# Kernel optimization log

Hardware: AMD Instinct MI355X
Metric: run time of the kernel (lower is better)

Reference implementation:

```python
import jax, jax.numpy as jnp
import numpy as np

B, NA, LD, AD = 2048, 8, 256, 256
D = LD + AD            # token_dim = 512
E, K, H = 4, 2, 8      # n_experts, top_k, n_attention_heads
FFN, HEAD, BINS = 2048, 512, 101
DH = D // H
LN_EPS = 1e-5


def setup_inputs() -> dict:
    key = jax.random.key(0)
    ks = jax.random.split(key, 9)
    s = 0.02
    return {
        "latents": jax.random.normal(ks[0], (B, NA, LD), jnp.float32),
        "actions": jax.random.normal(ks[1], (B, NA, AD), jnp.float32),
        "gate_W": jax.random.normal(ks[2], (NA * D, E), jnp.float32) * s,
        "Wqkv": jax.random.normal(ks[3], (E, D, 3 * D), jnp.float32) * s,
        "bqkv": jnp.zeros((E, 3 * D), jnp.float32),
        "Wo": jax.random.normal(ks[4], (E, D, D), jnp.float32) * s,
        "bo": jnp.zeros((E, D), jnp.float32),
        "ln1_g": jnp.ones((E, D), jnp.float32),
        "ln1_b": jnp.zeros((E, D), jnp.float32),
        "Wf1": jax.random.normal(ks[5], (E, D, FFN), jnp.float32) * s,
        "bf1": jnp.zeros((E, FFN), jnp.float32),
        "Wf2": jax.random.normal(ks[6], (E, FFN, D), jnp.float32) * s,
        "bf2": jnp.zeros((E, D), jnp.float32),
        "ln2_g": jnp.ones((E, D), jnp.float32),
        "ln2_b": jnp.zeros((E, D), jnp.float32),
        "head_W1": jax.random.normal(ks[7], (NA * D, HEAD), jnp.float32) * s,
        "head_b1": jnp.zeros((HEAD,), jnp.float32),
        "head_W2": jax.random.normal(ks[8], (HEAD, BINS), jnp.float32) * s,
        "head_b2": jnp.zeros((BINS,), jnp.float32),
    }


def _layernorm(x, g, b):
    mu = x.mean(-1, keepdims=True)
    var = ((x - mu) ** 2).mean(-1, keepdims=True)
    return (x - mu) / jnp.sqrt(var + LN_EPS) * g + b


def _expert(tokens, Wqkv, bqkv, Wo, bo, g1, b1, Wf1, bf1, Wf2, bf2, g2, b2):
    # tokens: [B, N, D] -> self-attention + FFN block (pre-residual, post-LN)
    b, n, d = tokens.shape
    qkv = tokens @ Wqkv + bqkv                                  # [B, N, 3D]
    q, k, v = jnp.split(qkv, 3, axis=-1)
    heads = lambda x: x.reshape(b, n, H, DH).transpose(0, 2, 1, 3)  # [B, H, N, dh]
    q, k, v = heads(q), heads(k), heads(v)
    scores = jnp.einsum("bhqd,bhkd->bhqk", q, k) / np.float32(np.sqrt(DH))
    attn = jax.nn.softmax(scores, axis=-1)
    ctx = jnp.einsum("bhqk,bhkd->bhqd", attn, v).transpose(0, 2, 1, 3).reshape(b, n, d)
    x = _layernorm(tokens + ctx @ Wo + bo, g1, b1)
    h = jax.nn.relu(x @ Wf1 + bf1) @ Wf2 + bf2
    return _layernorm(x + h, g2, b2)


def _cv2(x):
    # coefficient of variation squared (unbiased var, matches torch .var())
    x = x.astype(jnp.float32)
    return jnp.var(x, ddof=1) / (jnp.mean(x) ** 2 + 1e-10)


def reference(latents, actions, gate_W, Wqkv, bqkv, Wo, bo, ln1_g, ln1_b,
              Wf1, bf1, Wf2, bf2, ln2_g, ln2_b, head_W1, head_b1, head_W2, head_b2):
    tokens = jnp.concatenate([latents, actions], axis=-1)       # [B, NA, D]
    flat = tokens.reshape(B, -1)
    # --- router (eval mode: clean logits, no noise) ---
    logits = flat @ gate_W                                      # [B, E]
    topv, topi = jax.lax.top_k(logits, min(K + 1, E))
    gk = jax.nn.softmax(topv[:, :K], axis=1)
    gates = jnp.zeros_like(logits).at[jnp.arange(B)[:, None], topi[:, :K]].set(gk)
    # --- experts: run all densely; zero-gate tokens contribute nothing,
    #     identical math to the original masked dispatch/combine ---
    expert_out = jax.vmap(_expert, in_axes=(None,) + (0,) * 12)(
        tokens, Wqkv, bqkv, Wo, bo, ln1_g, ln1_b, Wf1, bf1, Wf2, bf2, ln2_g, ln2_b)  # [E, B, N, D]
    mixed = jnp.einsum("be,ebnd->bnd", gates, expert_out)
    reward_logits = jax.nn.relu(mixed.reshape(B, -1) @ head_W1 + head_b1) @ head_W2 + head_b2
    # --- aux: load balancing loss ---
    load = (gates > 0).sum(0)
    lbl = _cv2(gates.sum(0)) + _cv2(load) + jnp.mean(jax.nn.logsumexp(logits, axis=-1))
    return reward_logits, gates, lbl
```

## Files before the change

### kernel.cpp

```cpp
#include <hip/hip_runtime.h>
#include <stdint.h>

#define NB    2048
#define NAG   8
#define NEXP  4
#define LN_EPS 1e-5f

#define OUT_GATES  (2048*101)
#define OUT_LBL    (OUT_GATES + 2048*4)

typedef __attribute__((ext_vector_type(8))) short short8;
typedef __attribute__((ext_vector_type(4))) float f32x4;

#define MFMA_BF16(a,b,c) __builtin_amdgcn_mfma_f32_16x16x32_bf16((a),(b),(c),0,0,0)

__device__ __forceinline__ float bf2f(unsigned short h){
  union { unsigned int u; float f; } v; v.u = ((unsigned int)h) << 16; return v.f;
}
__device__ __forceinline__ unsigned short f2bf(float x){
  union { float f; unsigned int u; } v; v.f = x;
  unsigned int r = v.u + 0x7FFFu + ((v.u >> 16) & 1u);
  return (unsigned short)(r >> 16);
}
union bfpack8 { short8 v; unsigned short u[8]; };

__device__ __forceinline__ void gload16(const void* g, void* l){
  __builtin_amdgcn_global_load_lds(
      (const __attribute__((address_space(1))) void*)g,
      (__attribute__((address_space(3))) void*)l, 16, 0, 0);
}

#define OFF_WQKVT  0ULL
#define OFF_WOT    6291456ULL
#define OFF_WF1T   8388608ULL
#define OFF_WF2T   16777216ULL
#define OFF_HW1T   25165824ULL
#define OFF_HW2T   29360128ULL
#define OFF_XBF    29474816ULL
#define OFF_SLOTO  63029248ULL
#define OFF_HID    96583680ULL
#define OFF_JOBS   98680832ULL
#define OFF_SLOTW  98713600ULL
#define OFF_LSE    98729984ULL
#define OFF_CNT    98738176ULL
#define WS_NEED    98738192ULL

__global__ __launch_bounds__(256) void k_transpose_cast(const float* __restrict__ src,
    unsigned short* __restrict__ dst, int R, int C){
  __shared__ float tile[32][33];
  int e = blockIdx.z;
  int c0 = blockIdx.x*32, r0 = blockIdx.y*32;
  const float* s = src + (size_t)e*R*C;
  unsigned short* d = dst + (size_t)e*C*R;
  int tx = threadIdx.x & 31, ty = threadIdx.x >> 5;
  for(int yy = ty; yy < 32; yy += 8){
    int r = r0+yy, c = c0+tx;
    if(r<R && c<C) tile[yy][tx] = s[(size_t)r*C + c];
  }
  __syncthreads();
  for(int yy = ty; yy < 32; yy += 8){
    int oc = c0+yy, orr = r0+tx;
    if(oc<C && orr<R) d[(size_t)oc*R + orr] = f2bf(tile[tx][yy]);
  }
}

__global__ __launch_bounds__(256) void k_router(const float* __restrict__ lat,
    const float* __restrict__ act, const float* __restrict__ gateW,
    float* __restrict__ gates_out, int* __restrict__ jobs, int* __restrict__ cnt,
    float* __restrict__ slot_w, float* __restrict__ lse_arr){
  int b = blockIdx.x, t = threadIdx.x;
  float a0=0.f,a1=0.f,a2=0.f,a3=0.f;
  for(int i=t;i<4096;i+=256){
    int n=i>>9, d=i&511;
    float v = (d<256)? lat[((size_t)b*8+n)*256 + d] : act[((size_t)b*8+n)*256 + (d-256)];
    float4 gw = *(const float4*)&gateW[(size_t)i*4];
    a0 += v*gw.x; a1 += v*gw.y; a2 += v*gw.z; a3 += v*gw.w;
  }
  __shared__ float red[4][256];
  red[0][t]=a0; red[1][t]=a1; red[2][t]=a2; red[3][t]=a3;
  __syncthreads();
  for(int s=128;s>0;s>>=1){
    if(t<s){ red[0][t]+=red[0][t+s]; red[1][t]+=red[1][t+s]; red[2][t]+=red[2][t+s]; red[3][t]+=red[3][t+s]; }
    __syncthreads();
  }
  if(t==0){
    float lg[4] = {red[0][0], red[1][0], red[2][0], red[3][0]};
    int i1=0; for(int e=1;e<4;e++) if(lg[e]>lg[i1]) i1=e;
    int i2=-1; for(int e=0;e<4;e++){ if(e==i1) continue; if(i2<0 || lg[e]>lg[i2]) i2=e; }
    float m = lg[i1];
    float e2 = __expf(lg[i2]-m);
    float inv = 1.f/(1.f+e2);
    float w1 = inv, w2 = e2*inv;
    float g[4]={0.f,0.f,0.f,0.f}; g[i1]=w1; g[i2]=w2;
    gates_out[b*4+0]=g[0]; gates_out[b*4+1]=g[1]; gates_out[b*4+2]=g[2]; gates_out[b*4+3]=g[3];
    float s=0.f; for(int e=0;e<4;e++) s += __expf(lg[e]-m);
    lse_arr[b] = m + __logf(s);
    int p1 = atomicAdd(&cnt[i1],1); jobs[i1*2048+p1] = b*2+0; slot_w[b*2+0] = w1;
    int p2 = atomicAdd(&cnt[i2],1); jobs[i2*2048+p2] = b*2+1; slot_w[b*2+1] = w2;
  }
}

__global__ __launch_bounds__(256) void k_finalize(const float* __restrict__ gates,
    const float* __restrict__ lse_arr, const int* __restrict__ cnt, float* __restrict__ lbl){
  __shared__ float r0[256], r1[256], r2[256], r3[256], rl[256];
  int t = threadIdx.x;
  float g0=0.f,g1=0.f,g2=0.f,g3=0.f,l=0.f;
  for(int b=t;b<2048;b+=256){
    g0+=gates[b*4+0]; g1+=gates[b*4+1]; g2+=gates[b*4+2]; g3+=gates[b*4+3];
    l += lse_arr[b];
  }
  r0[t]=g0;r1[t]=g1;r2[t]=g2;r3[t]=g3;rl[t]=l;
  __syncthreads();
  for(int s=128;s>0;s>>=1){
    if(t<s){ r0[t]+=r0[t+s]; r1[t]+=r1[t+s]; r2[t]+=r2[t+s]; r3[t]+=r3[t+s]; rl[t]+=rl[t+s]; }
    __syncthreads();
  }
  if(t==0){
    float gs[4]={r0[0],r1[0],r2[0],r3[0]};
    float ld[4]={(float)cnt[0],(float)cnt[1],(float)cnt[2],(float)cnt[3]};
    float mu1=(gs[0]+gs[1]+gs[2]+gs[3])*0.25f;
    float v1=0.f; for(int i=0;i<4;i++){float d=gs[i]-mu1; v1+=d*d;} v1 *= (1.f/3.f);
    float mu2=(ld[0]+ld[1]+ld[2]+ld[3])*0.25f;
    float v2=0.f; for(int i=0;i<4;i++){float d=ld[i]-mu2; v2+=d*d;} v2 *= (1.f/3.f);
    lbl[0] = v1/(mu1*mu1+1e-10f) + v2/(mu2*mu2+1e-10f) + rl[0]*(1.f/2048.f);
  }
}

#define AT_LDS 158720
__global__ __launch_bounds__(512,2) void k_expert_attn(
    const float* __restrict__ lat, const float* __restrict__ act,
    const unsigned short* __restrict__ Wqkv_t, const float* __restrict__ bqkv,
    const unsigned short* __restrict__ Wo_t,   const float* __restrict__ bo,
    const float* __restrict__ ln1g, const float* __restrict__ ln1b,
    const int* __restrict__ jobs, const int* __restrict__ cnt,
    unsigned short* __restrict__ x_bf){
  extern __shared__ char smem[];
  char* Abase = smem;
  char* CTXb  = smem + 65536;
  char* U     = smem + 131072;
  float* SC   = (float*)(smem + 156672);

  int bid = blockIdx.x;
  int e   = (bid&7)>>1;
  int blk = ((bid>>3)<<1) | (bid&1);
  int ne = cnt[e];
  int base = blk*8;
  if(base >= ne) return;
  int t = threadIdx.x;
  int w = t>>6, lane = t&63, lg = lane>>4, lm = lane&15;
  int mt = w>>1, wb = w&1;
  const int* jb = &jobs[e*2048 + base];

  #pragma unroll
  for(int i=0;i<8;i++){
    int u = i*512 + t; int row = u>>6, ch = u&63; int d0 = ch*8;
    int j = row>>3;
    int slot = (base + j < ne) ? jb[j] : jb[0];
    int b = slot>>1, n = row&7;
    const float* src = (d0<256)? &lat[((size_t)b*8+n)*256 + d0]
                               : &act[((size_t)b*8+n)*256 + (d0-256)];
    float4 f0 = *(const float4*)src; float4 f1 = *(const float4*)(src+4);
    bfpack8 pk;
    pk.u[0]=f2bf(f0.x); pk.u[1]=f2bf(f0.y); pk.u[2]=f2bf(f0.z); pk.u[3]=f2bf(f0.w);
    pk.u[4]=f2bf(f1.x); pk.u[5]=f2bf(f1.y); pk.u[6]=f2bf(f1.z); pk.u[7]=f2bf(f1.w);
    *(short8*)(Abase + (((unsigned)(row*1024 + ch*16)) ^ ((unsigned)(row&7)<<4))) = pk.v;
  }

  const char* Wq = (const char*)(Wqkv_t + (size_t)e*1536*512);
  unsigned short* QH = (unsigned short*)U;

  for(int h=0; h<8; h++){
    f32x4 acc1[6];
    #pragma unroll
    for(int i=0;i<6;i++) acc1[i]=(f32x4){0.f,0.f,0.f,0.f};
    for(int ks=0; ks<8; ks++){
      __syncthreads();
      #pragma unroll
      for(int q=0;q<3;q++){
        unsigned L = (unsigned)w*3072u + (unsigned)q*1024u + (unsigned)lane*16u;
        int row = (int)(L>>7); unsigned pb = L & 127u;
        int gc = (row<64)? h*64+row : (row<128)? 512+h*64+(row-64) : 1024+h*64+(row-128);
        const char* g = Wq + (size_t)gc*1024 + ks*128 + (pb ^ ((unsigned)(row&7)<<4));
        gload16(g, U + ((unsigned)w*3072u + (unsigned)q*1024u));
      }
      __syncthreads();
      int arow = mt*16+lm;
      #pragma unroll
      for(int half=0; half<2; half++){
        short8 a = *(const short8*)(Abase + (unsigned)arow*1024u
                     + (((unsigned)(ks*128 + half*64 + lg*16)) ^ ((unsigned)(arow&7)<<4)));
        #pragma unroll
        for(int i=0;i<6;i++){
          int brow = (wb*6+i)*16+lm;
          short8 bb = *(const short8*)(U + (unsigned)brow*128u
                       + (((unsigned)(half*64+lg*16)) ^ ((unsigned)(brow&7)<<4)));
          acc1[i] = MFMA_BF16(a, bb, acc1[i]);
        }
      }
    }
    __syncthreads();
    #pragma unroll
    for(int i=0;i<6;i++){
      int L = (wb*6+i)*16 + lm;
      int gc = (L<64)? h*64+L : (L<128)? 512+h*64+(L-64) : 1024+h*64+(L-128);
      float bia = bqkv[e*1536 + gc];
      #pragma unroll
      for(int rr=0;rr<4;rr++){
        int row = mt*16 + lg*4 + rr;
        QH[row*200 + L] = f2bf(acc1[i][rr] + bia);
      }
    }
    __syncthreads();
    {
      int r = t>>3, p = t&7, j = r>>3;
      float s = 0.f;
      #pragma unroll
      for(int dd=0; dd<64; dd+=8){
        bfpack8 qa; qa.v = *(const short8*)&QH[r*200 + dd];
        bfpack8 ka; ka.v = *(const short8*)&QH[(j*8+p)*200 + 64 + dd];
        #pragma unroll
        for(int ii=0;ii<8;ii++) s += bf2f(qa.u[ii])*bf2f(ka.u[ii]);
      }
      SC[r*8+p] = s * 0.125f;
    }
    __syncthreads();
    {
      int r = t>>3, p = t&7, j = r>>3;
      float sv[8]; float m = -1e30f;
      #pragma unroll
      for(int kk=0;kk<8;kk++){ sv[kk]=SC[r*8+kk]; m = fmaxf(m, sv[kk]); }
      float ssum = 0.f;
      #pragma unroll
      for(int kk=0;kk<8;kk++){ sv[kk]=__expf(sv[kk]-m); ssum += sv[kk]; }
      float inv = 1.f/ssum;
      float o[8] = {0.f,0.f,0.f,0.f,0.f,0.f,0.f,0.f};
      #pragma unroll
      for(int kk=0;kk<8;kk++){
        float pr = sv[kk]*inv;
        bfpack8 va; va.v = *(const short8*)&QH[(j*8+kk)*200 + 128 + p*8];
        #pragma unroll
        for(int ii=0;ii<8;ii++) o[ii] += pr * bf2f(va.u[ii]);
      }
      bfpack8 pk;
      #pragma unroll
      for(int ii=0;ii<8;ii++) pk.u[ii]=f2bf(o[ii]);
      *(short8*)(CTXb + (((unsigned)(r*1024 + h*128 + p*16)) ^ ((unsigned)(r&7)<<4))) = pk.v;
    }
  }

  const char* WoP = (const char*)(Wo_t + (size_t)e*512*512);
  for(int nh=0; nh<4; nh++){
    f32x4 acc2[4];
    #pragma unroll
    for(int i=0;i<4;i++) acc2[i]=(f32x4){0.f,0.f,0.f,0.f};
    for(int ks=0; ks<8; ks++){
      __syncthreads();
      #pragma unroll
      for(int q=0;q<2;q++){
        unsigned L = (unsigned)w*2048u + (unsigned)q*1024u + (unsigned)lane*16u;
        int row = (int)(L>>7); unsigned pb = L&127u;
        const char* g = WoP + (size_t)(nh*128+row)*1024 + ks*128 + (pb ^ ((unsigned)(row&7)<<4));
        gload16(g, U + ((unsigned)w*2048u + (unsigned)q*1024u));
      }
      __syncthreads();
      int arow = mt*16+lm;
      #pragma unroll
      for(int half=0; half<2; half++){
        short8 a = *(const short8*)(CTXb + (unsigned)arow*1024u
                     + (((unsigned)(ks*128+half*64+lg*16)) ^ ((unsigned)(arow&7)<<4)));
        #pragma unroll
        for(int i=0;i<4;i++){
          int brow = (wb*4+i)*16+lm;
          short8 bb = *(const short8*)(U + (unsigned)brow*128u
                       + (((unsigned)(half*64+lg*16)) ^ ((unsigned)(brow&7)<<4)));
          acc2[i] = MFMA_BF16(a, bb, acc2[i]);
        }
      }
    }
    #pragma unroll
    for(int i=0;i<4;i++){
      int gcol = nh*128 + (wb*4+i)*16 + lm;
      float bia = bo[e*512 + gcol];
      #pragma unroll
      for(int rr=0;rr<4;rr++){
        int row = mt*16 + lg*4 + rr;
        int j2 = row>>3;
        int slot = (base+j2<ne)? jb[j2] : jb[0];
        int b = slot>>1, n = row&7;
        float tok = (gcol<256)? lat[((size_t)b*8+n)*256 + gcol]
                              : act[((size_t)b*8+n)*256 + gcol - 256];
        *(unsigned short*)(Abase + (((unsigned)(row*1024 + gcol*2)) ^ ((unsigned)(row&7)<<4)))
            = f2bf(acc2[i][rr] + bia + tok);
      }
    }
  }
  __syncthreads();
  {
    int r = t>>3, p = t&7;
    unsigned rsw = ((unsigned)(r&7))<<4;
    bfpack8 xv[8];
    float sum=0.f, sq=0.f;
    #pragma unroll
    for(int j=0;j<8;j++){
      xv[j].v = *(const short8*)(Abase + (((unsigned)(r*1024 + j*128 + p*16)) ^ rsw));
      #pragma unroll
      for(int ii=0;ii<8;ii++){ float f = bf2f(xv[j].u[ii]); sum += f; sq += f*f; }
    }
    sum += __shfl_xor(sum,1); sq += __shfl_xor(sq,1);
    sum += __shfl_xor(sum,2); sq += __shfl_xor(sq,2);
    sum += __shfl_xor(sum,4); sq += __shfl_xor(sq,4);
    float mu = sum*(1.f/512.f);
    float var = sq*(1.f/512.f) - mu*mu;
    float rstd = rsqrtf(var + LN_EPS);
    int j8 = r>>3;
    if(base + j8 < ne){
      int slot = jb[j8]; int n = r&7;
      unsigned short* dst = &x_bf[((size_t)slot*8+n)*512];
      #pragma unroll
      for(int j=0;j<8;j++){
        bfpack8 pk;
        #pragma unroll
        for(int ii=0;ii<8;ii++){
          int gc = j*64 + p*8 + ii;
          float xvv = (bf2f(xv[j].u[ii]) - mu)*rstd*ln1g[e*512+gc] + ln1b[e*512+gc];
          pk.u[ii] = f2bf(xvv);
        }
        *(short8*)&dst[j*64 + p*8] = pk.v;
      }
    }
  }
}

#define E2_LDS 99328
#define E2_HP  264

#define FFN_STAGE_W1(cc, kk, dst) do{ \
    const char* _Wb = W1 + ((size_t)(cc)*256)*1024; \
    unsigned _Lw = (unsigned)w*4096u; \
    _Pragma("unroll") \
    for(int _q=0;_q<4;_q++){ \
      unsigned _L = _Lw + (unsigned)_q*1024u + (unsigned)lane*16u; \
      int _row = (int)(_L>>7); unsigned _pb = _L&127u; \
      const char* _g = _Wb + (size_t)_row*1024 + (kk)*128 + (_pb ^ ((unsigned)(_row&7)<<4)); \
      gload16(_g, (dst) + (_Lw + (unsigned)_q*1024u)); \
    } }while(0)

#define FFN_STAGE_W2(cc, nn, kk, dst) do{ \
    unsigned _Lw = (unsigned)w*4096u; \
    _Pragma("unroll") \
    for(int _q=0;_q<4;_q++){ \
      unsigned _L = _Lw + (unsigned)_q*1024u + (unsigned)lane*16u; \
      int _row = (int)(_L>>7); unsigned _pb = _L&127u; \
      const char* _g = W2 + (size_t)((nn)*256+_row)*4096 + ((cc)*256+(kk)*64)*2 \
                     + (_pb ^ ((unsigned)(_row&7)<<4)); \
      gload16(_g, (dst) + (_Lw + (unsigned)_q*1024u)); \
    } }while(0)

__global__ __launch_bounds__(512,2) void k_expert_ffn(
    const unsigned short* __restrict__ x_bf,
    const unsigned short* __restrict__ Wf1_t, const float* __restrict__ bf1,
    const unsigned short* __restrict__ Wf2_t, const float* __restrict__ bf2v,
    const float* __restrict__ ln2g, const float* __restrict__ ln2b,
    const int* __restrict__ jobs, const int* __restrict__ cnt,
    unsigned short* __restrict__ slot_out){
  extern __shared__ char smem[];
  char* BSB0 = smem;
  char* BSB1 = smem + 32768;
  unsigned short* HC = (unsigned short*)(smem + 65536);
  unsigned short* PL = (unsigned short*)smem;

  int bid = blockIdx.x;
  int e   = (bid&7)>>1;
  int blk = ((bid>>3)<<1) | (bid&1);
  int ne = cnt[e];
  int base = blk*8;
  if(base >= ne) return;
  int t = threadIdx.x;
  int w = t>>6, lane = t&63, lg = lane>>4, lm = lane&15;
  int mg = w>>2, ng = w&3;
  const int* jb = &jobs[e*2048 + base];
  unsigned bswz = ((unsigned)(lm&7))<<4;

  const char* W1 = (const char*)(Wf1_t + (size_t)e*2048*512);
  const char* W2 = (const char*)(Wf2_t + (size_t)e*512*2048);

  const char* xb[2];
  #pragma unroll
  for(int ms=0;ms<2;ms++){
    int row = mg*32 + ms*16 + lm;
    int j = row>>3;
    int slot = (base+j<ne)? jb[j] : jb[0];
    int n = row&7;
    xb[ms] = (const char*)x_bf + (((size_t)slot*8+n)<<10) + (size_t)(lg*16);
  }

  short8 xf[2][2][2];
  #pragma unroll
  for(int ms=0;ms<2;ms++)
    #pragma unroll
    for(int hf=0;hf<2;hf++)
      xf[0][ms][hf] = *(const short8*)(xb[ms] + hf*64);

  f32x4 acc[2][2][4];
  #pragma unroll
  for(int a=0;a<2;a++)
    #pragma unroll
    for(int b=0;b<2;b++)
      #pragma unroll
      for(int c2=0;c2<4;c2++) acc[a][b][c2]=(f32x4){0.f,0.f,0.f,0.f};

  FFN_STAGE_W1(0, 0, BSB0);
  __syncthreads();

  for(int c=0; c<8; c++){
    f32x4 acc1[2][4];
    #pragma unroll
    for(int b=0;b<2;b++)
      #pragma unroll
      for(int c2=0;c2<4;c2++) acc1[b][c2]=(f32x4){0.f,0.f,0.f,0.f};

    #pragma unroll
    for(int ks=0; ks<8; ks++){
      char* nxt = ((ks+1)&1) ? BSB1 : BSB0;
      if(ks<7) FFN_STAGE_W1(c, ks+1, nxt);
      else     FFN_STAGE_W2(c, 0, 0, nxt);
      #pragma unroll
      for(int ms=0;ms<2;ms++)
        #pragma unroll
        for(int hf=0;hf<2;hf++)
          xf[(ks+1)&1][ms][hf] = *(const short8*)(xb[ms] + (((ks+1)&7)*128 + hf*64));
      const char* bs = (ks&1) ? BSB1 : BSB0;
      #pragma unroll
      for(int hf=0;hf<2;hf++){
        #pragma unroll
        for(int ns=0;ns<4;ns++){
          unsigned boff = (unsigned)(((ng*4+ns)*16+lm)*128);
          short8 bb = *(const short8*)(bs + boff + (((unsigned)(hf*64+lg*16)) ^ bswz));
          acc1[0][ns] = MFMA_BF16(xf[ks&1][0][hf], bb, acc1[0][ns]);
          acc1[1][ns] = MFMA_BF16(xf[ks&1][1][hf], bb, acc1[1][ns]);
        }
      }
      if(ks==7){
        #pragma unroll
        for(int ms=0;ms<2;ms++)
          #pragma unroll
          for(int ns=0;ns<4;ns++){
            int colL = ng*64 + ns*16 + lm;
            float bia = bf1[e*2048 + c*256 + colL];
            #pragma unroll
            for(int rr=0;rr<4;rr++){
              int row = mg*32 + ms*16 + lg*4 + rr;
              HC[row*E2_HP + colL] = f2bf(fmaxf(acc1[ms][ns][rr] + bia, 0.f));
            }
          }
      }
      __syncthreads();
    }

    #pragma unroll
    for(int s2=0; s2<8; s2++){
      const int nh = s2>>2, k2 = s2&3;
      char* nxt = ((s2+1)&1) ? BSB1 : BSB0;
      if(s2<7)      FFN_STAGE_W2(c, (s2+1)>>2, (s2+1)&3, nxt);
      else if(c<7)  FFN_STAGE_W1(c+1, 0, nxt);
      const char* bs = (s2&1) ? BSB1 : BSB0;
      #pragma unroll
      for(int hf=0;hf<2;hf++){
        short8 ha0 = *(const short8*)&HC[(mg*32 +      lm)*E2_HP + k2*64 + hf*32 + lg*8];
        short8 ha1 = *(const short8*)&HC[(mg*32 + 16 + lm)*E2_HP + k2*64 + hf*32 + lg*8];
        #pragma unroll
        for(int ns=0;ns<4;ns++){
          unsigned boff = (unsigned)(((ng*4+ns)*16+lm)*128);
          short8 bb = *(const short8*)(bs + boff + (((unsigned)(hf*64+lg*16)) ^ bswz));
          acc[nh][0][ns] = MFMA_BF16(ha0, bb, acc[nh][0][ns]);
          acc[nh][1][ns] = MFMA_BF16(ha1, bb, acc[nh][1][ns]);
        }
      }
      __syncthreads();
    }
  }

  #pragma unroll
  for(int nh=0;nh<2;nh++)
    #pragma unroll
    for(int ms=0;ms<2;ms++)
      #pragma unroll
      for(int ns=0;ns<4;ns++){
        int col = nh*256 + ng*64 + ns*16 + lm;
        float bia = bf2v[e*512+col];
        #pragma unroll
        for(int rr=0;rr<4;rr++){
          int row = mg*32 + ms*16 + lg*4 + rr;
          PL[row*520 + col] = f2bf(acc[nh][ms][ns][rr] + bia);
        }
      }
  __syncthreads();

  {
    int r = t>>3, p = t&7;
    int j8 = r>>3;
    int slot = (base + j8 < ne) ? jb[j8] : jb[0];
    int n = r&7;
    const unsigned short* xg = &x_bf[((size_t)slot*8+n)*512];
    bfpack8 cv[8];
    float sum=0.f, sq=0.f;
    #pragma unroll
    for(int j=0;j<8;j++){
      bfpack8 pa; pa.v = *(const short8*)&PL[r*520 + j*64 + p*8];
      bfpack8 xa; xa.v = *(const short8*)&xg[j*64 + p*8];
      #pragma unroll
      for(int ii=0;ii<8;ii++){
        float f = bf2f(pa.u[ii]) + bf2f(xa.u[ii]);
        cv[j].u[ii] = f2bf(f);
        f = bf2f(cv[j].u[ii]);
        sum += f; sq += f*f;
      }
    }
    sum += __shfl_xor(sum,1); sq += __shfl_xor(sq,1);
    sum += __shfl_xor(sum,2); sq += __shfl_xor(sq,2);
    sum += __shfl_xor(sum,4); sq += __shfl_xor(sq,4);
    float mu = sum*(1.f/512.f);
    float var = sq*(1.f/512.f) - mu*mu;
    float rstd = rsqrtf(var + LN_EPS);
    if(base + j8 < ne){
      unsigned short* dst = &slot_out[((size_t)slot*8+n)*512];
      #pragma unroll
      for(int j=0;j<8;j++){
        bfpack8 pk;
        #pragma unroll
        for(int ii=0;ii<8;ii++){
          int gc = j*64 + p*8 + ii;
          float xv = (bf2f(cv[j].u[ii]) - mu)*rstd*ln2g[e*512+gc] + ln2b[e*512+gc];
          pk.u[ii] = f2bf(xv);
        }
        *(short8*)&dst[j*64 + p*8] = pk.v;
      }
    }
  }
}

__global__ __launch_bounds__(256) void k_combine(const unsigned short* __restrict__ so,
    const float* __restrict__ slotw, unsigned short* __restrict__ mx){
  int gid = blockIdx.x*256 + threadIdx.x;
  int b = gid >> 9, c8 = gid & 511;
  float w0 = slotw[b*2+0], w1 = slotw[b*2+1];
  bfpack8 x0; x0.v = *(const short8*)&so[((size_t)(b*2+0))*4096 + c8*8];
  bfpack8 x1; x1.v = *(const short8*)&so[((size_t)(b*2+1))*4096 + c8*8];
  bfpack8 o;
  #pragma unroll
  for(int j=0;j<8;j++) o.u[j] = f2bf(w0*bf2f(x0.u[j]) + w1*bf2f(x1.u[j]));
  *(short8*)&mx[(size_t)b*4096 + c8*8] = o.v;
}

#define H_SP 72
__global__ __launch_bounds__(256) void k_head1(const unsigned short* __restrict__ mixbf,
    const unsigned short* __restrict__ hW1t, const float* __restrict__ b1,
    unsigned short* __restrict__ hidden){
  __shared__ unsigned short As[64*H_SP], Bs[64*H_SP];
  int n0 = blockIdx.x*64, m0 = blockIdx.y*64;
  int t = threadIdx.x, w = t>>6, lane = t&63, lg = lane>>4, lm = lane&15;
  f32x4 acc[4]; for(int i=0;i<4;i++) acc[i]=(f32x4){0.f,0.f,0.f,0.f};
  for(int ks=0; ks<64; ks++){
    __syncthreads();
    int k0 = ks*64;
    for(int i=0;i<2;i++){
      int u = i*256 + t; int row = u>>3, ch = u&7;
      *(short8*)&As[row*H_SP + ch*8] = *(const short8*)&mixbf[(size_t)(m0+row)*4096 + k0 + ch*8];
    }
    for(int i=0;i<2;i++){
      int u = i*256 + t; int row = u>>3, ch = u&7;
      *(short8*)&Bs[row*H_SP + ch*8] = *(const short8*)&hW1t[(size_t)(n0+row)*4096 + k0 + ch*8];
    }
    __syncthreads();
    for(int half=0; half<2; half++){
      short8 a = *(const short8*)&As[(w*16+lm)*H_SP + half*32 + lg*8];
      for(int i=0;i<4;i++){
        short8 bb = *(const short8*)&Bs[(i*16+lm)*H_SP + half*32 + lg*8];
        acc[i] = MFMA_BF16(a, bb, acc[i]);
      }
    }
  }
  for(int i=0;i<4;i++){
    int gc = n0 + i*16 + lm; float bia = b1[gc];
    for(int rr=0; rr<4; rr++){
      int row = m0 + w*16 + lg*4 + rr;
      hidden[(size_t)row*512 + gc] = f2bf(fmaxf(acc[i][rr] + bia, 0.f));
    }
  }
}

__global__ __launch_bounds__(256) void k_head2(const unsigned short* __restrict__ hidden,
    const unsigned short* __restrict__ hW2t, const float* __restrict__ b2,
    float* __restrict__ out){
  __shared__ unsigned short As[64*H_SP], Bs[112*H_SP];
  int m0 = blockIdx.x*64;
  int t = threadIdx.x, w = t>>6, lane = t&63, lg = lane>>4, lm = lane&15;
  f32x4 acc[7]; for(int i=0;i<7;i++) acc[i]=(f32x4){0.f,0.f,0.f,0.f};
  for(int ks=0; ks<8; ks++){
    __syncthreads();
    int k0 = ks*64;
    for(int i=0;i<2;i++){
      int u = i*256 + t; int row = u>>3, ch = u&7;
      *(short8*)&As[row*H_SP + ch*8] = *(const short8*)&hidden[(size_t)(m0+row)*512 + k0 + ch*8];
    }
    for(int i=0;i<4;i++){
      int u = i*256 + t;
      if(u < 896){
        int row = u>>3, ch = u&7;
        *(short8*)&Bs[row*H_SP + ch*8] = *(const short8*)&hW2t[(size_t)row*512 + k0 + ch*8];
      }
    }
    __syncthreads();
    for(int half=0; half<2; half++){
      short8 a = *(const short8*)&As[(w*16+lm)*H_SP + half*32 + lg*8];
      for(int i=0;i<7;i++){
        short8 bb = *(const short8*)&Bs[(i*16+lm)*H_SP + half*32 + lg*8];
        acc[i] = MFMA_BF16(a, bb, acc[i]);
      }
    }
  }
  for(int i=0;i<7;i++){
    int col = i*16 + lm;
    if(col < 101){
      float bia = b2[col];
      for(int rr=0; rr<4; rr++){
        int row = m0 + w*16 + lg*4 + rr;
        out[(size_t)row*101 + col] = acc[i][rr] + bia;
      }
    }
  }
}

extern "C" void kernel_launch(void* const* d_in, const int* in_sizes, int n_in,
                              void* d_out, int out_size, void* d_ws, size_t ws_size,
                              hipStream_t stream){
  if(ws_size < WS_NEED) return;
  const float* lat  = (const float*)d_in[0];
  const float* act  = (const float*)d_in[1];
  const float* gateW= (const float*)d_in[2];
  const float* Wqkv = (const float*)d_in[3];
  const float* bqkv = (const float*)d_in[4];
  const float* Wo   = (const float*)d_in[5];
  const float* bo   = (const float*)d_in[6];
  const float* ln1g = (const float*)d_in[7];
  const float* ln1b = (const float*)d_in[8];
  const float* Wf1  = (const float*)d_in[9];
  const float* bf1  = (const float*)d_in[10];
  const float* Wf2  = (const float*)d_in[11];
  const float* bf2v = (const float*)d_in[12];
  const float* ln2g = (const float*)d_in[13];
  const float* ln2b = (const float*)d_in[14];
  const float* hW1  = (const float*)d_in[15];
  const float* hb1  = (const float*)d_in[16];
  const float* hW2  = (const float*)d_in[17];
  const float* hb2  = (const float*)d_in[18];
  float* out = (float*)d_out;
  char* ws = (char*)d_ws;

  unsigned short* WQKVT = (unsigned short*)(ws + OFF_WQKVT);
  unsigned short* WOT   = (unsigned short*)(ws + OFF_WOT);
  unsigned short* WF1T  = (unsigned short*)(ws + OFF_WF1T);
  unsigned short* WF2T  = (unsigned short*)(ws + OFF_WF2T);
  unsigned short* HW1T  = (unsigned short*)(ws + OFF_HW1T);
  unsigned short* HW2T  = (unsigned short*)(ws + OFF_HW2T);
  unsigned short* XBF   = (unsigned short*)(ws + OFF_XBF);
  unsigned short* SLOTO = (unsigned short*)(ws + OFF_SLOTO);
  unsigned short* MIXBF = XBF;
  unsigned short* HID = (unsigned short*)(ws + OFF_HID);
  int* JOBS = (int*)(ws + OFF_JOBS);
  float* SLOTW = (float*)(ws + OFF_SLOTW);
  float* LSE = (float*)(ws + OFF_LSE);
  int* CNT = (int*)(ws + OFF_CNT);

  (void)hipFuncSetAttribute((const void*)k_expert_attn,
      hipFuncAttributeMaxDynamicSharedMemorySize, AT_LDS);
  (void)hipFuncSetAttribute((const void*)k_expert_ffn,
      hipFuncAttributeMaxDynamicSharedMemorySize, E2_LDS);

  hipMemsetAsync(CNT, 0, 16, stream);
  hipMemsetAsync(HW2T, 0, 112*512*2, stream);

  k_transpose_cast<<<dim3(48,16,4),256,0,stream>>>(Wqkv, WQKVT, 512, 1536);
  k_transpose_cast<<<dim3(16,16,4),256,0,stream>>>(Wo,   WOT,   512, 512);
  k_transpose_cast<<<dim3(64,16,4),256,0,stream>>>(Wf1,  WF1T,  512, 2048);
  k_transpose_cast<<<dim3(16,64,4),256,0,stream>>>(Wf2,  WF2T,  2048, 512);
  k_transpose_cast<<<dim3(16,128,1),256,0,stream>>>(hW1, HW1T,  4096, 512);
  k_transpose_cast<<<dim3(4,16,1),256,0,stream>>>(hW2,  HW2T,  512, 101);

  k_router<<<2048,256,0,stream>>>(lat, act, gateW, out + OUT_GATES, JOBS, CNT, SLOTW, LSE);
  k_finalize<<<1,256,0,stream>>>(out + OUT_GATES, LSE, CNT, out + OUT_LBL);

  k_expert_attn<<<1024, 512, AT_LDS, stream>>>(lat, act, WQKVT, bqkv, WOT, bo,
      ln1g, ln1b, JOBS, CNT, XBF);
  k_expert_ffn<<<1024, 512, E2_LDS, stream>>>(XBF, WF1T, bf1, WF2T, bf2v,
      ln2g, ln2b, JOBS, CNT, SLOTO);
  k_combine<<<4096,256,0,stream>>>(SLOTO, SLOTW, MIXBF);

  k_head1<<<dim3(8,32),256,0,stream>>>(MIXBF, HW1T, hb1, HID);
  k_head2<<<32,256,0,stream>>>(HID, HW2T, hb2, out);
}
```

Baseline: 898.2 us.

## Double-buffer weight staging in attention and FFN kernels with explicit vmcnt waits

Restructures the attention kernel so QKV and Wo weight tiles are double-buffered with prefetch of the next k-slice before computing the current one. The Wo projection is split into two head groups so the context buffer halves and LDS footprint shrinks. The FFN kernel replaces __syncthreads with raw barriers plus partial vmcnt waits so global-to-LDS loads stay in flight across iterations. This is meant to hide global load latency behind MFMA work, but it relies on hand-counted waitcnt values that are fragile and can break correctness if the counts are wrong.

New measurement: 811.6 us. 9.6% less time.

```diff
diff --git a/kernel.cpp b/kernel.cpp
--- a/kernel.cpp
+++ b/kernel.cpp
@@ -29,6 +29,10 @@
       (const __attribute__((address_space(1))) void*)g,
       (__attribute__((address_space(3))) void*)l, 16, 0, 0);
 }
+
+#define FBAR() do{ asm volatile("" ::: "memory"); \
+                   __builtin_amdgcn_s_barrier(); \
+                   asm volatile("" ::: "memory"); }while(0)
 
 #define OFF_WQKVT  0ULL
 #define OFF_WOT    6291456ULL
@@ -126,7 +130,29 @@
   }
 }
 
-#define AT_LDS 158720
+#define AT_LDS 149504
+
+#define STAGE_QKV(hh_, ks_, dst_) do{ \
+    _Pragma("unroll") \
+    for(int _q=0;_q<3;_q++){ \
+      unsigned _L = (unsigned)w*3072u + (unsigned)_q*1024u + (unsigned)lane*16u; \
+      int _row = (int)(_L>>7); unsigned _pb = _L & 127u; \
+      int _gc = (_row<64)? (hh_)*64+_row : (_row<128)? 512+(hh_)*64+(_row-64) : 1024+(hh_)*64+(_row-128); \
+      const char* _g = Wq + (size_t)_gc*1024 + (ks_)*128 + (_pb ^ ((unsigned)(_row&7)<<4)); \
+      gload16(_g, (dst_) + ((unsigned)w*3072u + (unsigned)_q*1024u)); \
+    } }while(0)
+
+#define STAGE_WO(hg_, s_, dst_) do{ \
+    int _nh = (s_)>>2, _k2 = (s_)&3; \
+    _Pragma("unroll") \
+    for(int _q=0;_q<2;_q++){ \
+      unsigned _L = (unsigned)w*2048u + (unsigned)_q*1024u + (unsigned)lane*16u; \
+      int _row = (int)(_L>>7); unsigned _pb = _L & 127u; \
+      const char* _g = WoP + (size_t)(_nh*128+_row)*1024 + (hg_)*512 + _k2*128 \
+                     + (_pb ^ ((unsigned)(_row&7)<<4)); \
+      gload16(_g, (dst_) + ((unsigned)w*2048u + (unsigned)_q*1024u)); \
+    } }while(0)
+
 __global__ __launch_bounds__(512,2) void k_expert_attn(
     const float* __restrict__ lat, const float* __restrict__ act,
     const unsigned short* __restrict__ Wqkv_t, const float* __restrict__ bqkv,
@@ -137,8 +163,8 @@
   extern __shared__ char smem[];
   char* Abase = smem;
   char* CTXb  = smem + 65536;
-  char* U     = smem + 131072;
-  float* SC   = (float*)(smem + 156672);
+  char* U     = smem + 98304;
+  float* SC   = (float*)(smem + 147456);
 
   int bid = blockIdx.x;
   int e   = (bid&7)>>1;
@@ -165,118 +191,128 @@
     pk.u[4]=f2bf(f1.x); pk.u[5]=f2bf(f1.y); pk.u[6]=f2bf(f1.z); pk.u[7]=f2bf(f1.w);
     *(short8*)(Abase + (((unsigned)(row*1024 + ch*16)) ^ ((unsigned)(row&7)<<4))) = pk.v;
   }
-
-  const char* Wq = (const char*)(Wqkv_t + (size_t)e*1536*512);
+  asm volatile("s_waitcnt lgkmcnt(0)" ::: "memory");
+
+  const char* Wq  = (const char*)(Wqkv_t + (size_t)e*1536*512);
+  const char* WoP = (const char*)(Wo_t   + (size_t)e*512*512);
   unsigned short* QH = (unsigned short*)U;
 
-  for(int h=0; h<8; h++){
-    f32x4 acc1[6];
-    #pragma unroll
-    for(int i=0;i<6;i++) acc1[i]=(f32x4){0.f,0.f,0.f,0.f};
-    for(int ks=0; ks<8; ks++){
+  f32x4 acc2[4][4];
+  #pragma unroll
+  for(int a=0;a<4;a++)
+    #pragma unroll
+    for(int b2=0;b2<4;b2++) acc2[a][b2]=(f32x4){0.f,0.f,0.f,0.f};
+
+  for(int hg=0; hg<2; hg++){
+    for(int hh=0; hh<4; hh++){
+      int h = hg*4 + hh;
+      f32x4 acc1[6];
+      #pragma unroll
+      for(int i=0;i<6;i++) acc1[i]=(f32x4){0.f,0.f,0.f,0.f};
+
+      STAGE_QKV(h, 0, U);
+      #pragma unroll
+      for(int ks=0; ks<8; ks++){
+        char* nxt = U + (((ks+1)&1) ? 24576u : 0u);
+        if(ks<7) STAGE_QKV(h, ks+1, nxt);
+        if(ks<7) asm volatile("s_waitcnt vmcnt(3)" ::: "memory");
+        else     asm volatile("s_waitcnt vmcnt(0)" ::: "memory");
+        FBAR();
+        const char* bs = U + ((ks&1) ? 24576u : 0u);
+        int arow = mt*16+lm;
+        #pragma unroll
+        for(int half=0; half<2; half++){
+          short8 a = *(const short8*)(Abase + (unsigned)arow*1024u
+                       + (((unsigned)(ks*128 + half*64 + lg*16)) ^ ((unsigned)(arow&7)<<4)));
+          #pragma unroll
+          for(int i=0;i<6;i++){
+            int brow = (wb*6+i)*16+lm;
+            short8 bb = *(const short8*)(bs + (unsigned)brow*128u
+                         + (((unsigned)(half*64+lg*16)) ^ ((unsigned)(brow&7)<<4)));
+            acc1[i] = MFMA_BF16(a, bb, acc1[i]);
+          }
+        }
+        FBAR();
+      }
+      #pragma unroll
+      for(int i=0;i<6;i++){
+        int L = (wb*6+i)*16 + lm;
+        int gc = (L<64)? h*64+L : (L<128)? 512+h*64+(L-64) : 1024+h*64+(L-128);
+        float bia = bqkv[e*1536 + gc];
+        #pragma unroll
+        for(int rr=0;rr<4;rr++){
+          int row = mt*16 + lg*4 + rr;
+          QH[row*200 + L] = f2bf(acc1[i][rr] + bia);
+        }
+      }
       __syncthreads();
-      #pragma unroll
-      for(int q=0;q<3;q++){
-        unsigned L = (unsigned)w*3072u + (unsigned)q*1024u + (unsigned)lane*16u;
-        int row = (int)(L>>7); unsigned pb = L & 127u;
-        int gc = (row<64)? h*64+row : (row<128)? 512+h*64+(row-64) : 1024+h*64+(row-128);
-        const char* g = Wq + (size_t)gc*1024 + ks*128 + (pb ^ ((unsigned)(row&7)<<4));
-        gload16(g, U + ((unsigned)w*3072u + (unsigned)q*1024u));
+      {
+        int r = t>>3, p = t&7, j = r>>3;
+        float s = 0.f;
+        #pragma unroll
+        for(int dd=0; dd<64; dd+=8){
+          bfpack8 qa; qa.v = *(const short8*)&QH[r*200 + dd];
+          bfpack8 ka; ka.v = *(const short8*)&QH[(j*8+p)*200 + 64 + dd];
+          #pragma unroll
+          for(int ii=0;ii<8;ii++) s += bf2f(qa.u[ii])*bf2f(ka.u[ii]);
+        }
+        SC[r*8+p] = s * 0.125f;
       }
       __syncthreads();
+      {
+        int r = t>>3, p = t&7, j = r>>3;
+        float sv[8]; float m = -1e30f;
+        #pragma unroll
+        for(int kk=0;kk<8;kk++){ sv[kk]=SC[r*8+kk]; m = fmaxf(m, sv[kk]); }
+        float ssum = 0.f;
+        #pragma unroll
+        for(int kk=0;kk<8;kk++){ sv[kk]=__expf(sv[kk]-m); ssum += sv[kk]; }
+        float inv = 1.f/ssum;
+        float o[8] = {0.f,0.f,0.f,0.f,0.f,0.f,0.f,0.f};
+        #pragma unroll
+        for(int kk=0;kk<8;kk++){
+          float pr = sv[kk]*inv;
+          bfpack8 va; va.v = *(const short8*)&QH[(j*8+kk)*200 + 128 + p*8];
+          #pragma unroll
+          for(int ii=0;ii<8;ii++) o[ii] += pr * bf2f(va.u[ii]);
+        }
+        bfpack8 pk;
+        #pragma unroll
+        for(int ii=0;ii<8;ii++) pk.u[ii]=f2bf(o[ii]);
+        *(short8*)(CTXb + (((unsigned)(r*512 + hh*128 + p*16)) ^ ((unsigned)(r&7)<<4))) = pk.v;
+      }
+      __syncthreads();
+    }
+
+    STAGE_WO(hg, 0, U);
+    #pragma unroll
+    for(int s=0; s<16; s++){
+      int nh = s>>2, k2 = s&3;
+      char* nxt = U + (((s+1)&1) ? 16384u : 0u);
+      if(s<15) STAGE_WO(hg, s+1, nxt);
+      if(s<15) asm volatile("s_waitcnt vmcnt(2)" ::: "memory");
+      else     asm volatile("s_waitcnt vmcnt(0)" ::: "memory");
+      FBAR();
+      const char* bs = U + ((s&1) ? 16384u : 0u);
       int arow = mt*16+lm;
       #pragma unroll
       for(int half=0; half<2; half++){
-        short8 a = *(const short8*)(Abase + (unsigned)arow*1024u
-                     + (((unsigned)(ks*128 + half*64 + lg*16)) ^ ((unsigned)(arow&7)<<4)));
-        #pragma unroll
-        for(int i=0;i<6;i++){
-          int brow = (wb*6+i)*16+lm;
-          short8 bb = *(const short8*)(U + (unsigned)brow*128u
-                       + (((unsigned)(half*64+lg*16)) ^ ((unsigned)(brow&7)<<4)));
-          acc1[i] = MFMA_BF16(a, bb, acc1[i]);
-        }
-      }
-    }
-    __syncthreads();
-    #pragma unroll
-    for(int i=0;i<6;i++){
-      int L = (wb*6+i)*16 + lm;
-      int gc = (L<64)? h*64+L : (L<128)? 512+h*64+(L-64) : 1024+h*64+(L-128);
-      float bia = bqkv[e*1536 + gc];
-      #pragma unroll
-      for(int rr=0;rr<4;rr++){
-        int row = mt*16 + lg*4 + rr;
-        QH[row*200 + L] = f2bf(acc1[i][rr] + bia);
-      }
-    }
-    __syncthreads();
-    {
-      int r = t>>3, p = t&7, j = r>>3;
-      float s = 0.f;
-      #pragma unroll
-      for(int dd=0; dd<64; dd+=8){
-        bfpack8 qa; qa.v = *(const short8*)&QH[r*200 + dd];
-        bfpack8 ka; ka.v = *(const short8*)&QH[(j*8+p)*200 + 64 + dd];
-        #pragma unroll
-        for(int ii=0;ii<8;ii++) s += bf2f(qa.u[ii])*bf2f(ka.u[ii]);
-      }
-      SC[r*8+p] = s * 0.125f;
-    }
-    __syncthreads();
-    {
-      int r = t>>3, p = t&7, j = r>>3;
-      float sv[8]; float m = -1e30f;
-      #pragma unroll
-      for(int kk=0;kk<8;kk++){ sv[kk]=SC[r*8+kk]; m = fmaxf(m, sv[kk]); }
-      float ssum = 0.f;
-      #pragma unroll
-      for(int kk=0;kk<8;kk++){ sv[kk]=__expf(sv[kk]-m); ssum += sv[kk]; }
-      float inv = 1.f/ssum;
-      float o[8] = {0.f,0.f,0.f,0.f,0.f,0.f,0.f,0.f};
-      #pragma unroll
-      for(int kk=0;kk<8;kk++){
-        float pr = sv[kk]*inv;
-        bfpack8 va; va.v = *(const short8*)&QH[(j*8+kk)*200 + 128 + p*8];
-        #pragma unroll
-        for(int ii=0;ii<8;ii++) o[ii] += pr * bf2f(va.u[ii]);
-      }
-      bfpack8 pk;
-      #pragma unroll
-      for(int ii=0;ii<8;ii++) pk.u[ii]=f2bf(o[ii]);
-      *(short8*)(CTXb + (((unsigned)(r*1024 + h*128 + p*16)) ^ ((unsigned)(r&7)<<4))) = pk.v;
-    }
-  }
-
-  const char* WoP = (const char*)(Wo_t + (size_t)e*512*512);
-  for(int nh=0; nh<4; nh++){
-    f32x4 acc2[4];
-    #pragma unroll
-    for(int i=0;i<4;i++) acc2[i]=(f32x4){0.f,0.f,0.f,0.f};
-    for(int ks=0; ks<8; ks++){
-      __syncthreads();
-      #pragma unroll
-      for(int q=0;q<2;q++){
-        unsigned L = (unsigned)w*2048u + (unsigned)q*1024u + (unsigned)lane*16u;
-        int row = (int)(L>>7); unsigned pb = L&127u;
-        const char* g = WoP + (size_t)(nh*128+row)*1024 + ks*128 + (pb ^ ((unsigned)(row&7)<<4));
-        gload16(g, U + ((unsigned)w*2048u + (unsigned)q*1024u));
-      }
-      __syncthreads();
-      int arow = mt*16+lm;
-      #pragma unroll
-      for(int half=0; half<2; half++){
-        short8 a = *(const short8*)(CTXb + (unsigned)arow*1024u
-                     + (((unsigned)(ks*128+half*64+lg*16)) ^ ((unsigned)(arow&7)<<4)));
+        short8 a = *(const short8*)(CTXb + (unsigned)arow*512u
+                     + (((unsigned)(k2*128 + half*64 + lg*16)) ^ ((unsigned)(arow&7)<<4)));
         #pragma unroll
         for(int i=0;i<4;i++){
           int brow = (wb*4+i)*16+lm;
-          short8 bb = *(const short8*)(U + (unsigned)brow*128u
+          short8 bb = *(const short8*)(bs + (unsigned)brow*128u
                        + (((unsigned)(half*64+lg*16)) ^ ((unsigned)(brow&7)<<4)));
-          acc2[i] = MFMA_BF16(a, bb, acc2[i]);
-        }
-      }
-    }
+          acc2[nh][i] = MFMA_BF16(a, bb, acc2[nh][i]);
+        }
+      }
+      FBAR();
+    }
+  }
+
+  #pragma unroll
+  for(int nh=0; nh<4; nh++)
     #pragma unroll
     for(int i=0;i<4;i++){
       int gcol = nh*128 + (wb*4+i)*16 + lm;
@@ -290,10 +326,9 @@
         float tok = (gcol<256)? lat[((size_t)b*8+n)*256 + gcol]
                               : act[((size_t)b*8+n)*256 + gcol - 256];
         *(unsigned short*)(Abase + (((unsigned)(row*1024 + gcol*2)) ^ ((unsigned)(row&7)<<4)))
-            = f2bf(acc2[i][rr] + bia + tok);
-      }
-    }
-  }
+            = f2bf(acc2[nh][i][rr] + bia + tok);
+      }
+    }
   __syncthreads();
   {
     int r = t>>3, p = t&7;
@@ -410,7 +445,6 @@
       for(int c2=0;c2<4;c2++) acc[a][b][c2]=(f32x4){0.f,0.f,0.f,0.f};
 
   FFN_STAGE_W1(0, 0, BSB0);
-  __syncthreads();
 
   for(int c=0; c<8; c++){
     f32x4 acc1[2][4];
@@ -421,14 +455,16 @@
 
     #pragma unroll
     for(int ks=0; ks<8; ks++){
+      #pragma unroll
+      for(int ms=0;ms<2;ms++)
+        #pragma unroll
+        for(int hf=0;hf<2;hf++)
+          xf[(ks+1)&1][ms][hf] = *(const short8*)(xb[ms] + (((ks+1)&7)*128 + hf*64));
       char* nxt = ((ks+1)&1) ? BSB1 : BSB0;
       if(ks<7) FFN_STAGE_W1(c, ks+1, nxt);
       else     FFN_STAGE_W2(c, 0, 0, nxt);
-      #pragma unroll
-      for(int ms=0;ms<2;ms++)
-        #pragma unroll
-        for(int hf=0;hf<2;hf++)
-          xf[(ks+1)&1][ms][hf] = *(const short8*)(xb[ms] + (((ks+1)&7)*128 + hf*64));
+      asm volatile("s_waitcnt vmcnt(8)" ::: "memory");
+      FBAR();
       const char* bs = (ks&1) ? BSB1 : BSB0;
       #pragma unroll
       for(int hf=0;hf<2;hf++){
@@ -453,8 +489,9 @@
               HC[row*E2_HP + colL] = f2bf(fmaxf(acc1[ms][ns][rr] + bia, 0.f));
             }
           }
-      }
-      __syncthreads();
+        asm volatile("s_waitcnt lgkmcnt(0)" ::: "memory");
+      }
+      FBAR();
     }
 
     #pragma unroll
@@ -463,6 +500,13 @@
       char* nxt = ((s2+1)&1) ? BSB1 : BSB0;
       if(s2<7)      FFN_STAGE_W2(c, (s2+1)>>2, (s2+1)&3, nxt);
       else if(c<7)  FFN_STAGE_W1(c+1, 0, nxt);
+      if(s2<7){
+        asm volatile("s_waitcnt vmcnt(4)" ::: "memory");
+      } else {
+        if(c<7) asm volatile("s_waitcnt vmcnt(4)" ::: "memory");
+        else    asm volatile("s_waitcnt vmcnt(0)" ::: "memory");
+      }
+      FBAR();
       const char* bs = (s2&1) ? BSB1 : BSB0;
       #pragma unroll
       for(int hf=0;hf<2;hf++){
@@ -476,7 +520,7 @@
           acc[nh][1][ns] = MFMA_BF16(ha1, bb, acc[nh][1][ns]);
         }
       }
-      __syncthreads();
+      FBAR();
     }
   }
 
```
